# Kernel optimization log

Measured on AMD Instinct MI355X. Metric: run time of the kernel, lower is better.

The kernel has to match this reference:

```python
import jax, jax.numpy as jnp
import numpy as np

CH = (16, 32, 16)
T_STEPS = 30
THRESH = 1.0


def conv3d(x, w, b):
    # x: (B, Cin, D, H, W), w: (Cout, Cin, kD, kH, kW), stride 2, VALID
    y = jax.lax.conv_general_dilated(
        x, w, window_strides=(2, 2, 2), padding='VALID',
        dimension_numbers=('NCDHW', 'OIDHW', 'NCDHW'))
    return y + b[None, :, None, None, None]


def setup_inputs() -> dict:
    key = jax.random.key(0)
    ks = jax.random.split(key, 11)
    B = 4
    x = jax.random.normal(ks[0], (B, 24, 602, 602), jnp.float32)

    def uinit(k, shape, fan_in):
        bound = 1.0 / np.sqrt(fan_in)
        return jax.random.uniform(k, shape, jnp.float32, -bound, bound)

    fan1 = 1 * 3 * 15 * 15
    fan2 = CH[0] * 3 * 15 * 15
    fan3 = CH[1] * 3 * 15 * 15
    w1 = uinit(ks[1], (CH[0], 1, 3, 15, 15), fan1)
    b1 = uinit(ks[2], (CH[0],), fan1)
    w2 = uinit(ks[3], (CH[1], CH[0], 3, 15, 15), fan2)
    b2 = uinit(ks[4], (CH[1],), fan2)
    w3 = uinit(ks[5], (CH[2], CH[1], 3, 15, 15), fan3)
    b3 = uinit(ks[6], (CH[2],), fan3)
    F1 = 21632 * CH[2] // 16  # 21632 for CH[2]=16
    fc1_w = uinit(ks[7], (512, F1), F1)
    fc1_b = uinit(ks[8], (512,), F1)
    fc2_w = uinit(ks[9], (54, 512), 512)
    fc2_b = uinit(ks[10], (54,), 512)
    return dict(x=x, w1=w1, b1=b1, w2=w2, b2=b2, w3=w3, b3=b3,
                fc1_w=fc1_w, fc1_b=fc1_b, fc2_w=fc2_w, fc2_b=fc2_b)


def _forward(x, w1, b1, w2, b2, w3, b3, fc1_w, fc1_b, fc2_w, fc2_b):
    B = x.shape[0]
    # avg_pool2d(kernel=2): (B,24,602,602) -> (B,24,301,301)
    xp = x.reshape(B, 24, 301, 2, 301, 2).mean(axis=(3, 5))
    h = xp[:, None]  # (B,1,24,301,301)
    h = jax.nn.relu(conv3d(h, w1, b1))  # (B,16,11,144,144)
    h = jax.nn.relu(conv3d(h, w2, b2))  # (B,32,5,65,65)
    h = jax.nn.relu(conv3d(h, w3, b3))  # (B,16,2,26,26)
    x_snn = h.reshape(B, -1)            # (B, 21632)

    sgn = jnp.sign(x_snn)
    prob = jnp.abs(x_snn) * 0.5

    def step(carry, k):
        m0, m1 = carry
        r = jax.random.uniform(k, x_snn.shape, x_snn.dtype)
        # Poisson encoding with straight-through gradient to x_snn
        spikes = (prob > r).astype(x_snn.dtype) * sgn
        p_in = jax.lax.stop_gradient(spikes - x_snn) + x_snn
        m0 = m0 + p_in @ fc1_w.T + fc1_b
        # LIF: threshold, subtract, spike with surrogate (pass-through where fired)
        fire = m0 > THRESH
        ex = jnp.where(fire, m0, 0.0)
        m0 = m0 - ex
        out = jnp.where(fire, ex - jax.lax.stop_gradient(ex) + 1.0, 0.0)
        m1 = m1 + out @ fc2_w.T + fc2_b
        return (m0, m1), None

    keys = jax.random.split(jax.random.key(42), T_STEPS)
    init = (jnp.zeros((B, 512), x_snn.dtype), jnp.zeros((B, 54), x_snn.dtype))
    (_, m1), _ = jax.lax.scan(step, init, keys)
    return m1


def reference(x, w1, b1, w2, b2, w3, b3, fc1_w, fc1_b, fc2_w, fc2_b):
    return _forward(x, w1, b1, w2, b2, w3, b3, fc1_w, fc1_b, fc2_w, fc2_b)
```

## Files before the change

kernel.cpp:

```cpp
#include <hip/hip_runtime.h>
#include <stdint.h>

struct SnnKeys { unsigned int k0[30]; unsigned int k1[30]; };

__host__ __device__ static inline void tf2x32(unsigned int k0, unsigned int k1,
                                              unsigned int& x0, unsigned int& x1) {
  unsigned int ks2 = k0 ^ k1 ^ 0x1BD11BDAu;
#define TF_RND(r) { x0 += x1; x1 = (x1 << (r)) | (x1 >> (32 - (r))); x1 ^= x0; }
  x0 += k0; x1 += k1;
  TF_RND(13) TF_RND(15) TF_RND(26) TF_RND(6)
  x0 += k1; x1 += ks2 + 1u;
  TF_RND(17) TF_RND(29) TF_RND(16) TF_RND(24)
  x0 += ks2; x1 += k0 + 2u;
  TF_RND(13) TF_RND(15) TF_RND(26) TF_RND(6)
  x0 += k0; x1 += k1 + 3u;
  TF_RND(17) TF_RND(29) TF_RND(16) TF_RND(24)
  x0 += k1; x1 += ks2 + 4u;
  TF_RND(13) TF_RND(15) TF_RND(26) TF_RND(6)
  x0 += ks2; x1 += k0 + 5u;
#undef TF_RND
}

#define POOL_N (4 * 24 * 301 * 301)

__global__ __launch_bounds__(256) void k_pool(const float* __restrict__ x,
                                              float* __restrict__ xp) {
  int i = blockIdx.x * 256 + threadIdx.x;
  if (i >= POOL_N) return;
  int j = i % 301;
  int rest = i / 301;
  int r = rest % 301;
  int bc = rest / 301;
  const float* src = x + ((size_t)bc * 602 + 2 * r) * 602 + 2 * j;
  float2 a = *(const float2*)src;
  float2 b = *(const float2*)(src + 602);
  xp[i] = 0.25f * ((a.x + a.y) + (b.x + b.y));
}

__global__ __launch_bounds__(256) void k_wt2(const float* __restrict__ w2,
                                             float* __restrict__ w2t) {
  int i = blockIdx.x * 256 + threadIdx.x;
  if (i >= 345600) return;
  int co = i & 31;
  int rest = i >> 5;
  int ci = rest / 675;
  int k675 = rest - ci * 675;
  w2t[i] = w2[((size_t)co * 16 + ci) * 675 + k675];
}

__global__ __launch_bounds__(256) void k_wt3(const float* __restrict__ w3,
                                             float* __restrict__ w3t) {
  int i = blockIdx.x * 256 + threadIdx.x;
  if (i >= 345600) return;
  int co = i & 15;
  int rest = i >> 4;
  int ci = rest / 675;
  int k675 = rest - ci * 675;
  w3t[i] = w3[((size_t)co * 32 + ci) * 675 + k675];
}

__global__ __launch_bounds__(256) void k_conv1(const float* __restrict__ xp,
                                               const float* __restrict__ w1,
                                               const float* __restrict__ b1,
                                               float* __restrict__ h1) {
  __shared__ alignas(16) float in_e[25 * 152];
  __shared__ alignas(16) float in_o[25 * 152];
  const int tid = threadIdx.x;
  const int wave = __builtin_amdgcn_readfirstlane(tid >> 6);
  const int lane = tid & 63;
  const int cog = wave >> 1, sg = wave & 1;
  const int cob = cog * 8;
  const int bz = blockIdx.y;
  const int b = bz / 11, d = bz % 11;
  const int s0 = blockIdx.x * 512;
  const int y0 = s0 / 144;

  int sq[4], be[4];
  bool vq[4];
#pragma unroll
  for (int q = 0; q < 4; ++q) {
    int s = s0 + sg * 256 + q * 64 + lane;
    vq[q] = (s < 20736);
    int sc = vq[q] ? s : 20735;
    int y = sc / 144, xx = sc - y * 144;
    sq[q] = s;
    be[q] = 2 * (y - y0) * 152 + xx;
  }

  float acc[8][4] = {};

  for (int kd = 0; kd < 3; ++kd) {
    __syncthreads();
    const int din = 2 * d + kd;
    const float* src = xp + (size_t)(b * 24 + din) * 90601;
    for (int i = tid; i < 25 * 301; i += 256) {
      int r = i / 301, c = i - r * 301;
      int gr = 2 * y0 + r;
      float v = (gr < 301) ? src[gr * 301 + c] : 0.0f;
      ((c & 1) ? in_o : in_e)[r * 152 + (c >> 1)] = v;
    }
    __syncthreads();
    const float* wp = w1 + cob * 675 + kd * 225;
    for (int kh = 0; kh < 15; ++kh) {
      float e[4][8], o[4][7];
#pragma unroll
      for (int q = 0; q < 4; ++q) {
        const float* pe = in_e + be[q] + kh * 152;
        const float* po = in_o + be[q] + kh * 152;
#pragma unroll
        for (int j = 0; j < 8; ++j) e[q][j] = pe[j];
#pragma unroll
        for (int j = 0; j < 7; ++j) o[q][j] = po[j];
      }
      const float* wk = wp + kh * 15;
#pragma unroll
      for (int j = 0; j < 8; ++j) {
#pragma unroll
        for (int c = 0; c < 8; ++c) {
          float wv = wk[c * 675 + 2 * j];
#pragma unroll
          for (int q = 0; q < 4; ++q) acc[c][q] += wv * e[q][j];
        }
      }
#pragma unroll
      for (int j = 0; j < 7; ++j) {
#pragma unroll
        for (int c = 0; c < 8; ++c) {
          float wv = wk[c * 675 + 2 * j + 1];
#pragma unroll
          for (int q = 0; q < 4; ++q) acc[c][q] += wv * o[q][j];
        }
      }
    }
  }
#pragma unroll
  for (int q = 0; q < 4; ++q) {
    if (vq[q]) {
#pragma unroll
      for (int c = 0; c < 8; ++c) {
        float v = acc[c][q] + b1[cob + c];
        h1[((size_t)(b * 16 + cob + c) * 11 + d) * 20736 + sq[q]] = fmaxf(v, 0.0f);
      }
    }
  }
}

__global__ __launch_bounds__(256) void k_conv2(const float* __restrict__ h1,
                                               const float* __restrict__ w2t,
                                               float* __restrict__ h2p) {
  __shared__ alignas(16) float in_e[23 * 76];
  __shared__ alignas(16) float in_o[23 * 76];
  const int tid = threadIdx.x;
  const int wave = __builtin_amdgcn_readfirstlane(tid >> 6);
  const int lane = tid & 63;
  const int cob = wave * 8;
  const int bz = blockIdx.y;
  const int cig3 = bz % 3;
  const int t5 = bz / 3;
  const int b = t5 / 5, d = t5 % 5;
  const int g0 = blockIdx.x * 64;
  const int r0 = g0 / 17;
  const int row0 = 2 * r0;

  const int gi0 = g0 + lane;
  const bool valid = (gi0 < 1105);
  const int gi = valid ? gi0 : 1104;
  const int r = gi / 17;
  const int g = gi - r * 17;
  const int lr = r - r0;
  const int x0 = g * 4;

  float acc[8][4] = {};

  for (int s = 0; s < 16; ++s) {
    const int u = cig3 * 16 + s;
    const int ci = u / 3;
    const int kd = u - 3 * ci;
    __syncthreads();
    const int din = 2 * d + kd;
    const float* src = h1 + (size_t)((b * 16 + ci) * 11 + din) * 20736;
    for (int i = tid; i < 23 * 36; i += 256) {
      int irr = i / 36, c4 = i - irr * 36;
      int gr = row0 + irr;
      float4 v = {0.0f, 0.0f, 0.0f, 0.0f};
      if (gr < 144) v = *(const float4*)(src + gr * 144 + c4 * 4);
      *(float2*)&in_e[irr * 76 + 2 * c4] = make_float2(v.x, v.z);
      *(float2*)&in_o[irr * 76 + 2 * c4] = make_float2(v.y, v.w);
    }
    __syncthreads();
    const float* wkb = w2t + (size_t)(ci * 3 + kd) * 225 * 32 + cob;
    const float* pe0 = in_e + 2 * lr * 76 + x0;
    const float* po0 = in_o + 2 * lr * 76 + x0;
#pragma unroll 5
    for (int kh = 0; kh < 15; ++kh) {
      float4 e0 = *(const float4*)(pe0 + kh * 76);
      float4 e1 = *(const float4*)(pe0 + kh * 76 + 4);
      float4 e2 = *(const float4*)(pe0 + kh * 76 + 8);
      float4 o0 = *(const float4*)(po0 + kh * 76);
      float4 o1 = *(const float4*)(po0 + kh * 76 + 4);
      float4 o2 = *(const float4*)(po0 + kh * 76 + 8);
      float E[12] = {e0.x, e0.y, e0.z, e0.w, e1.x, e1.y, e1.z, e1.w,
                     e2.x, e2.y, e2.z, e2.w};
      float O[12] = {o0.x, o0.y, o0.z, o0.w, o1.x, o1.y, o1.z, o1.w,
                     o2.x, o2.y, o2.z, o2.w};
      const float* wk = wkb + kh * 480;
#pragma unroll
      for (int m = 0; m < 8; ++m) {
#pragma unroll
        for (int c = 0; c < 8; ++c) {
          float wv = wk[m * 64 + c];
#pragma unroll
          for (int u2 = 0; u2 < 4; ++u2) acc[c][u2] += wv * E[m + u2];
        }
      }
#pragma unroll
      for (int m = 0; m < 7; ++m) {
#pragma unroll
        for (int c = 0; c < 8; ++c) {
          float wv = wk[m * 64 + 32 + c];
#pragma unroll
          for (int u2 = 0; u2 < 4; ++u2) acc[c][u2] += wv * O[m + u2];
        }
      }
    }
  }
  if (valid) {
    float* dst = h2p + (size_t)cig3 * 2704000 +
                 ((size_t)(b * 32 + cob) * 5 + d) * 4225 + r * 65 + x0;
#pragma unroll
    for (int c = 0; c < 8; ++c) {
#pragma unroll
      for (int u = 0; u < 4; ++u) {
        if (x0 + u < 65) dst[(size_t)c * 21125 + u] = acc[c][u];
      }
    }
  }
}

__global__ __launch_bounds__(256) void k_h2fix(const float* __restrict__ p,
                                               const float* __restrict__ b2,
                                               float* __restrict__ h2) {
  int i = blockIdx.x * 256 + threadIdx.x;
  if (i >= 2704000) return;
  int co = (i / 21125) & 31;
  float v = p[i] + p[2704000 + i] + p[5408000 + i] + b2[co];
  h2[i] = fmaxf(v, 0.0f);
}

__global__ __launch_bounds__(256) void k_conv3(const float* __restrict__ h2,
                                               const float* __restrict__ w3t,
                                               float* __restrict__ h3p) {
  __shared__ alignas(16) float in_e[55 * 36];
  __shared__ alignas(16) float in_o[55 * 36];
  const int tid = threadIdx.x;
  const int wave = __builtin_amdgcn_readfirstlane(tid >> 6);
  const int lane = tid & 63;
  const int cog = wave >> 1, sg = wave & 1;
  const int cob = cog * 8;
  const int bz = blockIdx.y;
  const int b = bz >> 1, d = bz & 1;
  const int ci = blockIdx.z;
  const int s0 = blockIdx.x * 512;
  const int y0 = s0 / 26;

  int sq[4], be[4];
  bool vq[4];
#pragma unroll
  for (int q = 0; q < 4; ++q) {
    int s = s0 + sg * 256 + q * 64 + lane;
    vq[q] = (s < 676);
    int sc = vq[q] ? s : 675;
    int y = sc / 26, xx = sc - y * 26;
    sq[q] = s;
    be[q] = 2 * (y - y0) * 36 + xx;
  }

  float acc[8][4] = {};

  for (int kd = 0; kd < 3; ++kd) {
    __syncthreads();
    const int din = 2 * d + kd;
    const float* src = h2 + (size_t)((b * 32 + ci) * 5 + din) * 4225;
    for (int i = tid; i < 55 * 65; i += 256) {
      int r = i / 65, c = i - r * 65;
      int gr = 2 * y0 + r;
      float v = (gr < 65) ? src[gr * 65 + c] : 0.0f;
      ((c & 1) ? in_o : in_e)[r * 36 + (c >> 1)] = v;
    }
    __syncthreads();
    const float* wkbase = w3t + (size_t)(ci * 3 + kd) * 225 * 16 + cob;
    for (int kh = 0; kh < 15; ++kh) {
      float e[4][8], o[4][7];
#pragma unroll
      for (int q = 0; q < 4; ++q) {
        const float* pe = in_e + be[q] + kh * 36;
        const float* po = in_o + be[q] + kh * 36;
#pragma unroll
        for (int j = 0; j < 8; ++j) e[q][j] = pe[j];
#pragma unroll
        for (int j = 0; j < 7; ++j) o[q][j] = po[j];
      }
      const float* wr = wkbase + kh * 15 * 16;
#pragma unroll
      for (int j = 0; j < 8; ++j) {
#pragma unroll
        for (int c = 0; c < 8; ++c) {
          float wv = wr[(2 * j) * 16 + c];
#pragma unroll
          for (int q = 0; q < 4; ++q) acc[c][q] += wv * e[q][j];
        }
      }
#pragma unroll
      for (int j = 0; j < 7; ++j) {
#pragma unroll
        for (int c = 0; c < 8; ++c) {
          float wv = wr[(2 * j + 1) * 16 + c];
#pragma unroll
          for (int q = 0; q < 4; ++q) acc[c][q] += wv * o[q][j];
        }
      }
    }
  }
#pragma unroll
  for (int q = 0; q < 4; ++q) {
    if (vq[q]) {
#pragma unroll
      for (int c = 0; c < 8; ++c) {
        h3p[(size_t)ci * 86528 +
            ((size_t)(b * 16 + cob + c) * 2 + d) * 676 + sq[q]] = acc[c][q];
      }
    }
  }
}

__global__ __launch_bounds__(256) void k_h3fix(const float* __restrict__ h3p,
                                               const float* __restrict__ b3,
                                               float* __restrict__ prob) {
  int p = blockIdx.x * 256 + threadIdx.x;
  if (p >= 86528) return;
  int co = (p % 21632) / 1352;
  float x = b3[co];
  for (int g = 0; g < 32; ++g) x += h3p[(size_t)g * 86528 + p];
  prob[p] = 0.5f * fmaxf(x, 0.0f);
}

__global__ __launch_bounds__(256) void k_spike(const float* __restrict__ prob,
                                               float* __restrict__ spk,
                                               SnnKeys keys) {
  int p = blockIdx.x * 256 + threadIdx.x;
  int t = blockIdx.y;
  float pr = prob[p];
  unsigned int x0 = 0u, x1 = (unsigned int)p;
  tf2x32(keys.k0[t], keys.k1[t], x0, x1);
  unsigned int bits = x0 ^ x1;
  float r = __uint_as_float((bits >> 9) | 0x3f800000u) - 1.0f;
  spk[(size_t)t * 86528 + p] = (pr > r) ? 1.0f : 0.0f;
}

__global__ __launch_bounds__(128) void k_fc1(const float* __restrict__ spk,
                                             const float* __restrict__ fc1w,
                                             float* __restrict__ incp) {
  __shared__ alignas(16) float slds[16][128];
  __shared__ alignas(16) float wlds[16][32];
  const int tx = threadIdx.x;
  const int ty = threadIdx.y;
  const int tid = ty * 8 + tx;
  const int nt = blockIdx.x;
  const int kc = blockIdx.y;
  const int k0base = kc * 832;

  float acc[8][4];
#pragma unroll
  for (int mi = 0; mi < 8; ++mi)
#pragma unroll
    for (int ni = 0; ni < 4; ++ni) acc[mi][ni] = 0.0f;

  for (int kb = 0; kb < 832; kb += 16) {
    const int k0 = k0base + kb;
    __syncthreads();
    {
      int m = tid;
      float4 v[4] = {{0,0,0,0},{0,0,0,0},{0,0,0,0},{0,0,0,0}};
      if (m < 120) {
        const float4* s = (const float4*)(spk + (size_t)m * 21632 + k0);
        v[0] = s[0]; v[1] = s[1]; v[2] = s[2]; v[3] = s[3];
      }
#pragma unroll
      for (int q = 0; q < 4; ++q) {
        slds[4 * q + 0][m] = v[q].x;
        slds[4 * q + 1][m] = v[q].y;
        slds[4 * q + 2][m] = v[q].z;
        slds[4 * q + 3][m] = v[q].w;
      }
    }
    for (int e = tid; e < 512; e += 128) {
      int n = e >> 4, kk = e & 15;
      wlds[kk][n] = fc1w[(size_t)(nt * 32 + n) * 21632 + k0 + kk];
    }
    __syncthreads();
#pragma unroll
    for (int kk = 0; kk < 16; ++kk) {
      const float4 wv = *(const float4*)&wlds[kk][tx * 4];
      const float4 s0 = *(const float4*)&slds[kk][ty * 8];
      const float4 s1 = *(const float4*)&slds[kk][ty * 8 + 4];
      float sv[8] = {s0.x, s0.y, s0.z, s0.w, s1.x, s1.y, s1.z, s1.w};
      float wz[4] = {wv.x, wv.y, wv.z, wv.w};
#pragma unroll
      for (int mi = 0; mi < 8; ++mi)
#pragma unroll
        for (int ni = 0; ni < 4; ++ni) acc[mi][ni] += sv[mi] * wz[ni];
    }
  }
#pragma unroll
  for (int mi = 0; mi < 8; ++mi) {
    int m = ty * 8 + mi;
    if (m < 120) {
      float4 o = {acc[mi][0], acc[mi][1], acc[mi][2], acc[mi][3]};
      *(float4*)&incp[((size_t)kc * 120 + m) * 512 + nt * 32 + tx * 4] = o;
    }
  }
}

__global__ __launch_bounds__(256) void k_scan(const float* __restrict__ incp,
                                              const float* __restrict__ fc1b,
                                              float* __restrict__ cnt) {
  int i = blockIdx.x * 256 + threadIdx.x;
  int b = i >> 9, n = i & 511;
  float bias = fc1b[n];
  float m0 = 0.0f, c = 0.0f;
  for (int t = 0; t < 30; ++t) {
    int m = t * 4 + b;
    float s = bias;
    for (int kc = 0; kc < 26; ++kc) s += incp[((size_t)kc * 120 + m) * 512 + n];
    m0 += s;
    if (m0 > 1.0f) { c += 1.0f; m0 = 0.0f; }
  }
  cnt[i] = c;
}

__global__ __launch_bounds__(256) void k_final(const float* __restrict__ cnt,
                                               const float* __restrict__ fc2w,
                                               const float* __restrict__ fc2b,
                                               float* __restrict__ out) {
  int o = threadIdx.x;
  if (o >= 216) return;
  int b = o / 54, oo = o - b * 54;
  const float* w = fc2w + (size_t)oo * 512;
  const float* c = cnt + (size_t)b * 512;
  float s = 0.0f;
  for (int n = 0; n < 512; ++n) s += c[n] * w[n];
  out[o] = s + 30.0f * fc2b[oo];
}

extern "C" void kernel_launch(void* const* d_in, const int* in_sizes, int n_in,
                              void* d_out, int out_size, void* d_ws, size_t ws_size,
                              hipStream_t stream) {
  (void)in_sizes; (void)n_in; (void)out_size; (void)ws_size;
  const float* x    = (const float*)d_in[0];
  const float* w1   = (const float*)d_in[1];
  const float* b1   = (const float*)d_in[2];
  const float* w2   = (const float*)d_in[3];
  const float* b2   = (const float*)d_in[4];
  const float* w3   = (const float*)d_in[5];
  const float* b3   = (const float*)d_in[6];
  const float* fc1w = (const float*)d_in[7];
  const float* fc1b = (const float*)d_in[8];
  const float* fc2w = (const float*)d_in[9];
  const float* fc2b = (const float*)d_in[10];
  float* out = (float*)d_out;
  float* ws  = (float*)d_ws;

  float* xp   = ws;
  float* h1   = ws + 8697696;
  float* w2t  = ws + 8112000;
  float* h2p  = ws;
  float* h2   = ws + 8697696;
  float* w3t  = ws;
  float* h3p  = ws + 11401696;
  float* prob = ws + 14170592;
  float* spk  = ws + 14257120;
  float* incp = ws + 16852960;
  float* cnt  = ws + 18450400;

  SnnKeys keys;
  for (int t = 0; t < 30; ++t) {
    unsigned int a = 0u, bb = (unsigned int)t;
    tf2x32(0u, 42u, a, bb);
    keys.k0[t] = a; keys.k1[t] = bb;
  }

  k_pool <<<(POOL_N + 255) / 256, 256, 0, stream>>>(x, xp);
  k_conv1<<<dim3(41, 44),    256, 0, stream>>>(xp, w1, b1, h1);
  k_wt2  <<<1350, 256, 0, stream>>>(w2, w2t);
  k_conv2<<<dim3(18, 60),    256, 0, stream>>>(h1, w2t, h2p);
  k_h2fix<<<(2704000 + 255) / 256, 256, 0, stream>>>(h2p, b2, h2);
  k_wt3  <<<1350, 256, 0, stream>>>(w3, w3t);
  k_conv3<<<dim3(2, 8, 32),  256, 0, stream>>>(h2, w3t, h3p);
  k_h3fix<<<338, 256, 0, stream>>>(h3p, b3, prob);
  k_spike<<<dim3(338, 30),   256, 0, stream>>>(prob, spk, keys);
  k_fc1  <<<dim3(16, 26), dim3(8, 16), 0, stream>>>(spk, fc1w, incp);
  k_scan <<<8, 256, 0, stream>>>(incp, fc1b, cnt);
  k_final<<<1, 256, 0, stream>>>(cnt, fc2w, fc2b, out);
}
```

Baseline: 1.562 ms.

## Double-buffer conv2 input tiles with register prefetch to overlap loads and compute

The conv2 kernel now keeps two LDS buffers and prefetches the next input slice into registers before computing on the current one. After the compute it writes the slice into the other buffer, so each stage needs one barrier instead of two. This hides global load latency behind the FMA loop, at the cost of 16 more registers per thread and twice the LDS, which could reduce occupancy.

```diff
diff --git a/kernel.cpp b/kernel.cpp
--- a/kernel.cpp
+++ b/kernel.cpp
@@ -148,8 +148,8 @@
 __global__ __launch_bounds__(256) void k_conv2(const float* __restrict__ h1,
                                                const float* __restrict__ w2t,
                                                float* __restrict__ h2p) {
-  __shared__ alignas(16) float in_e[23 * 76];
-  __shared__ alignas(16) float in_o[23 * 76];
+  __shared__ alignas(16) float in_e[2][23 * 76];
+  __shared__ alignas(16) float in_o[2][23 * 76];
   const int tid = threadIdx.x;
   const int wave = __builtin_amdgcn_readfirstlane(tid >> 6);
   const int lane = tid & 63;
@@ -171,26 +171,55 @@
   const int x0 = g * 4;
 
   float acc[8][4] = {};
-
-  for (int s = 0; s < 16; ++s) {
-    const int u = cig3 * 16 + s;
+  float4 pre[4];
+
+  auto issue = [&](int st) {
+    const int u = cig3 * 16 + st;
     const int ci = u / 3;
     const int kd = u - 3 * ci;
-    __syncthreads();
     const int din = 2 * d + kd;
     const float* src = h1 + (size_t)((b * 16 + ci) * 11 + din) * 20736;
-    for (int i = tid; i < 23 * 36; i += 256) {
-      int irr = i / 36, c4 = i - irr * 36;
-      int gr = row0 + irr;
+#pragma unroll
+    for (int ii = 0; ii < 4; ++ii) {
+      int i = tid + ii * 256;
       float4 v = {0.0f, 0.0f, 0.0f, 0.0f};
-      if (gr < 144) v = *(const float4*)(src + gr * 144 + c4 * 4);
-      *(float2*)&in_e[irr * 76 + 2 * c4] = make_float2(v.x, v.z);
-      *(float2*)&in_o[irr * 76 + 2 * c4] = make_float2(v.y, v.w);
-    }
-    __syncthreads();
+      if (i < 828) {
+        int irr = i / 36, c4 = i - irr * 36;
+        int gr = row0 + irr;
+        if (gr < 144) v = *(const float4*)(src + gr * 144 + c4 * 4);
+      }
+      pre[ii] = v;
+    }
+  };
+
+  auto write_lds = [&](int buf) {
+#pragma unroll
+    for (int ii = 0; ii < 4; ++ii) {
+      int i = tid + ii * 256;
+      if (i < 828) {
+        int irr = i / 36, c4 = i - irr * 36;
+        int off = irr * 76 + 2 * c4;
+        float4 v = pre[ii];
+        *(float2*)&in_e[buf][off] = make_float2(v.x, v.z);
+        *(float2*)&in_o[buf][off] = make_float2(v.y, v.w);
+      }
+    }
+  };
+
+  issue(0);
+  write_lds(0);
+  __syncthreads();
+
+  for (int st = 0; st < 16; ++st) {
+    const int cur = st & 1;
+    if (st < 15) issue(st + 1);
+
+    const int u = cig3 * 16 + st;
+    const int ci = u / 3;
+    const int kd = u - 3 * ci;
     const float* wkb = w2t + (size_t)(ci * 3 + kd) * 225 * 32 + cob;
-    const float* pe0 = in_e + 2 * lr * 76 + x0;
-    const float* po0 = in_o + 2 * lr * 76 + x0;
+    const float* pe0 = &in_e[cur][2 * lr * 76 + x0];
+    const float* po0 = &in_o[cur][2 * lr * 76 + x0];
 #pragma unroll 5
     for (int kh = 0; kh < 15; ++kh) {
       float4 e0 = *(const float4*)(pe0 + kh * 76);
@@ -222,6 +251,10 @@
           for (int u2 = 0; u2 < 4; ++u2) acc[c][u2] += wv * O[m + u2];
         }
       }
+    }
+    if (st < 15) {
+      write_lds(cur ^ 1);
+      __syncthreads();
     }
   }
   if (valid) {
```

New measurement: 1.998 ms. 1.28x slower.
